# Performance work log

Hardware: AMD Instinct MI355X
Metric: run time of the kernel (lower is better)

## Reference

```python
import jax, jax.numpy as jnp
import numpy as np
from jax import lax

CHUNK = 64
EPS = 1e-5


def chunk_gla(q, k, v, g, chunk=CHUNK):
    """Gated linear attention, chunked parallel form (scale=1, as in HGRN2).
    q,k,g: [B,H,L,DK]; v: [B,H,L,DV]; g is per-step log decay on key dims.
    Recurrence: S_t = diag(exp(g_t)) S_{t-1} + k_t^T v_t ; o_t = q_t S_t.
    """
    B, H, L, DK = q.shape
    DV = v.shape[-1]
    n = L // chunk
    qc = q.reshape(B, H, n, chunk, DK)
    kc = k.reshape(B, H, n, chunk, DK)
    vc = v.reshape(B, H, n, chunk, DV)
    gc = jnp.cumsum(g.reshape(B, H, n, chunk, DK), axis=3)   # inclusive cumsum of log decays
    g_last = gc[..., -1:, :]                                 # [B,H,n,1,DK] total chunk decay

    qg = qc * jnp.exp(gc)                 # decay-weighted queries
    kg = kc * jnp.exp(g_last - gc)        # keys scaled to end-of-chunk
    kd = kc * jnp.exp(-gc)                # keys unscaled for intra-chunk attn

    # intra-chunk causal attention
    A = jnp.einsum('bhntd,bhnsd->bhnts', qg, kd)
    mask = jnp.tril(jnp.ones((chunk, chunk), dtype=bool))
    A = jnp.where(mask, A, 0.0)
    o_intra = jnp.einsum('bhnts,bhnsd->bhntd', A, vc)

    # inter-chunk recurrence over n chunks
    def step(S, inp):
        qg_c, kg_c, vc_c, gl_c = inp  # [B,H,C,DK], [B,H,C,DK], [B,H,C,DV], [B,H,DK]
        o = jnp.einsum('bhtd,bhdv->bhtv', qg_c, S)
        S = S * jnp.exp(gl_c)[..., None] + jnp.einsum('bhtd,bhtv->bhdv', kg_c, vc_c)
        return S, o

    S0 = jnp.zeros((B, H, DK, DV), q.dtype)
    xs = (jnp.moveaxis(qg, 2, 0), jnp.moveaxis(kg, 2, 0),
          jnp.moveaxis(vc, 2, 0), jnp.moveaxis(g_last[..., 0, :], 2, 0))
    _, o_inter = lax.scan(step, S0, xs)   # [n,B,H,C,DV]
    o = o_intra + jnp.moveaxis(o_inter, 0, 2)
    return o.reshape(B, H, L, DV)


def rms_norm(x, w, eps=EPS):
    var = jnp.mean(jnp.square(x), axis=-1, keepdims=True)
    return x * lax.rsqrt(var + eps) * w


def setup_inputs() -> dict:
    key = jax.random.key(0)
    B, L, D = 4, 2048, 2048
    ks = jax.random.split(key, 6)
    s = 1.0 / np.sqrt(D)
    return {
        'x': jax.random.normal(ks[0], (B, L, D), jnp.float32),
        'Wq': jax.random.normal(ks[1], (D, D), jnp.float32) * s,
        'Wf': jax.random.normal(ks[2], (D, D), jnp.float32) * s,
        'Wi': jax.random.normal(ks[3], (D, D), jnp.float32) * s,
        'Wo': jax.random.normal(ks[4], (D, D), jnp.float32) * s,
        'gnorm_w': jnp.ones((D,), jnp.float32),
    }


def reference(x, Wq, Wf, Wi, Wo, gnorm_w):
    B, L, D = x.shape
    H = 16
    Dh = D // H

    q = jax.nn.sigmoid(x @ Wq.T)
    f = jax.nn.sigmoid(x @ Wf.T)
    i = x @ Wi.T
    k = 1.0 - f
    g = jnp.log(f)

    def split_heads(t):  # b l (h d) -> b h l d
        return t.reshape(B, L, H, Dh).transpose(0, 2, 1, 3)

    q, k, i, g = map(split_heads, (q, k, i, g))
    o = chunk_gla(q, k, i, g)                  # [B,H,L,Dh]
    o = o.transpose(0, 2, 1, 3).reshape(B, L, D)
    o = rms_norm(o, gnorm_w)
    return o @ Wo.T
```

## Files before the change

kernel.cpp:

```cpp
#include <hip/hip_runtime.h>
#include <math.h>

typedef __bf16 bf16_t;
typedef __bf16 bf16x8 __attribute__((ext_vector_type(8)));
typedef float  f32x4  __attribute__((ext_vector_type(4)));

__device__ __forceinline__ void gl2lds16(const void* g, void* l) {
  __builtin_amdgcn_global_load_lds((__attribute__((address_space(1))) void*)g,
                                   (__attribute__((address_space(3))) void*)l,
                                   16, 0, 0);
}

template<int MODE>
__global__ __launch_bounds__(256, 2)
void gemm_bt(const bf16_t* __restrict__ A, const bf16_t* __restrict__ B,
             void* __restrict__ out0, float* __restrict__ out1,
             int M, int N, int K)
{
  __shared__ __align__(16) bf16_t As[128 * 32];
  __shared__ __align__(16) bf16_t Bs[128 * 32];
  const int tt   = threadIdx.x;
  const int wave = tt >> 6;
  const int lane = tt & 63;
  const int nblk = N >> 7;
  const int m0 = (int)(blockIdx.x / nblk) * 128;
  const int n0 = (int)(blockIdx.x % nblk) * 128;
  const int wr = (wave >> 1) * 64;
  const int wc = (wave & 1) * 64;
  const int r  = lane & 15;
  const int ko = (lane >> 4) * 8;
  const int c0 = tt, c1 = tt + 256;
  const int ar0 = c0 >> 2, ac0 = (c0 & 3) * 8;
  const int ar1 = c1 >> 2, ac1 = (c1 & 3) * 8;

  f32x4 acc[4][4] = {};

  for (int kt = 0; kt < K; kt += 32) {
    gl2lds16(A + (size_t)(m0 + ar0) * K + kt + ac0, (void*)(As + wave * 512));
    gl2lds16(A + (size_t)(m0 + ar1) * K + kt + ac1, (void*)(As + 2048 + wave * 512));
    gl2lds16(B + (size_t)(n0 + ar0) * K + kt + ac0, (void*)(Bs + wave * 512));
    gl2lds16(B + (size_t)(n0 + ar1) * K + kt + ac1, (void*)(Bs + 2048 + wave * 512));
    asm volatile("s_waitcnt vmcnt(0)" ::: "memory");
    __syncthreads();
    bf16x8 a[4], b[4];
    #pragma unroll
    for (int i = 0; i < 4; i++) a[i] = *(const bf16x8*)(As + (wr + i * 16 + r) * 32 + ko);
    #pragma unroll
    for (int i = 0; i < 4; i++) b[i] = *(const bf16x8*)(Bs + (wc + i * 16 + r) * 32 + ko);
    #pragma unroll
    for (int i = 0; i < 4; i++)
      #pragma unroll
      for (int j = 0; j < 4; j++)
        acc[i][j] = __builtin_amdgcn_mfma_f32_16x16x32_bf16(a[i], b[j], acc[i][j], 0, 0, 0);
    __syncthreads();
  }

  #pragma unroll
  for (int i = 0; i < 4; i++)
    #pragma unroll
    for (int j = 0; j < 4; j++)
      #pragma unroll
      for (int jj = 0; jj < 4; jj++) {
        const int gr = m0 + wr + i * 16 + (lane >> 4) * 4 + jj;
        const int gc = n0 + wc + j * 16 + r;
        const size_t off = (size_t)gr * N + gc;
        const float v = acc[i][j][jj];
        if (MODE == 0) {
          ((bf16_t*)out0)[off] = (bf16_t)(1.0f / (1.0f + expf(-v)));
        } else if (MODE == 1) {
          ((bf16_t*)out0)[off] = (bf16_t)(1.0f / (1.0f + expf(v)));
          out1[off] = fminf(v, 0.0f) - log1pf(expf(-fabsf(v)));
        } else if (MODE == 2) {
          ((bf16_t*)out0)[off] = (bf16_t)v;
        } else {
          ((float*)out0)[off] = v;
        }
      }
}

__global__ void f2b_kernel(const float* __restrict__ in, bf16_t* __restrict__ out, int n8)
{
  const int idx = blockIdx.x * 256 + threadIdx.x;
  if (idx >= n8) return;
  const float4 a = *(const float4*)(in + (size_t)idx * 8);
  const float4 b = *(const float4*)(in + (size_t)idx * 8 + 4);
  bf16x8 o;
  o[0] = (bf16_t)a.x; o[1] = (bf16_t)a.y; o[2] = (bf16_t)a.z; o[3] = (bf16_t)a.w;
  o[4] = (bf16_t)b.x; o[5] = (bf16_t)b.y; o[6] = (bf16_t)b.z; o[7] = (bf16_t)b.w;
  *(bf16x8*)(out + (size_t)idx * 8) = o;
}

__global__ __launch_bounds__(256)
void prep2_kernel(bf16_t* __restrict__ qb, bf16_t* __restrict__ kb,
                  const float* __restrict__ g32, float* __restrict__ eglh)
{
  __shared__ __align__(16) float gs[64][132];
  __shared__ float gls[128];
  const int blk = blockIdx.x;
  const int c = blk & 31, h = (blk >> 5) & 15, b = blk >> 9;
  const size_t row0 = (size_t)b * 2048 + (size_t)c * 64;
  const int col0 = h * 128;
  const int tt = threadIdx.x;

  #pragma unroll
  for (int s = 0; s < 8; s++) {
    const int u = tt + s * 256;
    const int t = u >> 5, d4 = (u & 31) * 4;
    *(float4*)&gs[t][d4] = *(const float4*)(g32 + (row0 + t) * 2048 + col0 + d4);
  }
  __syncthreads();
  if (tt < 128) {
    float run = 0.0f;
    for (int t = 0; t < 64; t++) { run += gs[t][tt]; gs[t][tt] = run; }
    gls[tt] = 0.5f * run;
    eglh[(size_t)blk * 128 + tt] = expf(0.5f * run);
  }
  __syncthreads();
  #pragma unroll
  for (int s = 0; s < 4; s++) {
    const int u = tt + s * 256;
    const int t = u >> 4, d8 = (u & 15) * 8;
    bf16_t* qp = qb + (row0 + t) * 2048 + col0 + d8;
    bf16_t* kp = kb + (row0 + t) * 2048 + col0 + d8;
    const bf16x8 q8 = *(const bf16x8*)qp;
    const bf16x8 k8 = *(const bf16x8*)kp;
    bf16x8 qo, ko2;
    #pragma unroll
    for (int j = 0; j < 8; j++) {
      const float gc = gs[t][d8 + j];
      const float gh = gls[d8 + j];
      qo[j]  = (bf16_t)((float)q8[j] * expf(gc - gh));
      ko2[j] = (bf16_t)((float)k8[j] * expf(gh - gc));
    }
    *(bf16x8*)qp = qo;
    *(bf16x8*)kp = ko2;
  }
}

__global__ __launch_bounds__(256)
void state2_kernel(const bf16_t* __restrict__ kb, const bf16_t* __restrict__ vb,
                   const float* __restrict__ eglh, bf16_t* __restrict__ ST)
{
  __shared__ __align__(16) bf16_t kgt[64][72];
  __shared__ __align__(16) bf16_t vt[64][72];
  __shared__ float ehs[64];
  const int blk = blockIdx.x;
  const int dh = blk & 1, eh = (blk >> 1) & 1, bh = blk >> 2;
  const int b = bh >> 4, h = bh & 15;
  const int col0 = h * 128;
  const int tt = threadIdx.x, wave = tt >> 6, lane = tt & 63;
  const int r = lane & 15, ko = (lane >> 4) * 8;
  const int d0 = dh * 64, e0 = eh * 64;
  f32x4 acc[4] = {};

  for (int c = 0; c < 32; c++) {
    const size_t cb = (size_t)bh * 32 + c;
    const size_t row0 = (size_t)b * 2048 + (size_t)c * 64;
    if (tt < 64) ehs[tt] = eglh[cb * 128 + d0 + tt];
    __syncthreads();
    #pragma unroll
    for (int s = 0; s < 2; s++) {
      const int u = tt + s * 256;
      const int t = u >> 3, d8 = (u & 7) * 8;
      const bf16x8 kv = *(const bf16x8*)(kb + (row0 + t) * 2048 + col0 + d0 + d8);
      const bf16x8 vv = *(const bf16x8*)(vb + (row0 + t) * 2048 + col0 + e0 + d8);
      #pragma unroll
      for (int j = 0; j < 8; j++) {
        kgt[d8 + j][t] = (bf16_t)((float)kv[j] * ehs[d8 + j]);
        vt[d8 + j][t]  = vv[j];
      }
    }
    __syncthreads();
    #pragma unroll
    for (int nf = 0; nf < 4; nf++) {
      const int d = nf * 16 + r;
      const float sd = ehs[d];
      #pragma unroll
      for (int jj = 0; jj < 4; jj++) {
        const int e = e0 + wave * 16 + (lane >> 4) * 4 + jj;
        ST[(cb * 128 + e) * 128 + d0 + d] = (bf16_t)(acc[nf][jj] * sd);
      }
    }
    #pragma unroll
    for (int nf = 0; nf < 4; nf++) {
      const float ev = ehs[nf * 16 + r];
      const float e2 = ev * ev;
      #pragma unroll
      for (int jj = 0; jj < 4; jj++) acc[nf][jj] *= e2;
    }
    #pragma unroll
    for (int ks = 0; ks < 2; ks++) {
      const bf16x8 a = *(const bf16x8*)&vt[wave * 16 + r][ks * 32 + ko];
      #pragma unroll
      for (int nf = 0; nf < 4; nf++) {
        const bf16x8 bfr = *(const bf16x8*)&kgt[nf * 16 + r][ks * 32 + ko];
        acc[nf] = __builtin_amdgcn_mfma_f32_16x16x32_bf16(a, bfr, acc[nf], 0, 0, 0);
      }
    }
    __syncthreads();
  }
}

__global__ __launch_bounds__(256)
void chunk2_kernel(const bf16_t* __restrict__ qb, const bf16_t* __restrict__ kb,
                   const bf16_t* __restrict__ vb, const bf16_t* __restrict__ ST,
                   bf16_t* __restrict__ o16)
{
  __shared__ __align__(16) bf16_t qgs[64][136];
  __shared__ __align__(16) bf16_t kds[64][136];
  __shared__ __align__(16) bf16_t vTs[128][72];
  __shared__ __align__(16) bf16_t Ps[64][72];
  const int blk = blockIdx.x;
  const int c = blk & 31, h = (blk >> 5) & 15, b = blk >> 9;
  const size_t row0 = (size_t)b * 2048 + (size_t)c * 64;
  const int col0 = h * 128;
  const int tt = threadIdx.x, wave = tt >> 6, lane = tt & 63;
  const int r = lane & 15, ko = (lane >> 4) * 8;

  #pragma unroll
  for (int s = 0; s < 4; s++) {
    const int u = tt + s * 256;
    const int t = u >> 4, d8 = (u & 15) * 8;
    *(bf16x8*)&qgs[t][d8] = *(const bf16x8*)(qb + (row0 + t) * 2048 + col0 + d8);
    *(bf16x8*)&kds[t][d8] = *(const bf16x8*)(kb + (row0 + t) * 2048 + col0 + d8);
  }
  #pragma unroll
  for (int s = 0; s < 4; s++) {
    const int u = tt + s * 256;
    const int t = u >> 4, e8 = (u & 15) * 8;
    const bf16x8 vv = *(const bf16x8*)(vb + (row0 + t) * 2048 + col0 + e8);
    #pragma unroll
    for (int j = 0; j < 8; j++) vTs[e8 + j][t] = vv[j];
  }
  __syncthreads();

  bf16x8 aq[4];
  #pragma unroll
  for (int ks = 0; ks < 4; ks++) aq[ks] = *(const bf16x8*)&qgs[wave * 16 + r][ks * 32 + ko];

  f32x4 accA[4] = {};
  #pragma unroll
  for (int ks = 0; ks < 4; ks++)
    #pragma unroll
    for (int sf = 0; sf < 4; sf++) {
      const bf16x8 bfr = *(const bf16x8*)&kds[sf * 16 + r][ks * 32 + ko];
      accA[sf] = __builtin_amdgcn_mfma_f32_16x16x32_bf16(aq[ks], bfr, accA[sf], 0, 0, 0);
    }

  #pragma unroll
  for (int sf = 0; sf < 4; sf++)
    #pragma unroll
    for (int jj = 0; jj < 4; jj++) {
      const int t = wave * 16 + (lane >> 4) * 4 + jj;
      const int s = sf * 16 + r;
      Ps[t][s] = (bf16_t)(t >= s ? accA[sf][jj] : 0.0f);
    }

  f32x4 acc[8] = {};
  const size_t stbase = (size_t)blk * 128 * 128;
  #pragma unroll
  for (int ks = 0; ks < 4; ks++)
    #pragma unroll
    for (int ne = 0; ne < 8; ne++) {
      const bf16x8 bfr = *(const bf16x8*)(ST + stbase + (size_t)(ne * 16 + r) * 128 + ks * 32 + ko);
      acc[ne] = __builtin_amdgcn_mfma_f32_16x16x32_bf16(aq[ks], bfr, acc[ne], 0, 0, 0);
    }
  #pragma unroll
  for (int ks = 0; ks < 2; ks++) {
    const bf16x8 pa = *(const bf16x8*)&Ps[wave * 16 + r][ks * 32 + ko];
    #pragma unroll
    for (int ne = 0; ne < 8; ne++) {
      const bf16x8 bfr = *(const bf16x8*)&vTs[ne * 16 + r][ks * 32 + ko];
      acc[ne] = __builtin_amdgcn_mfma_f32_16x16x32_bf16(pa, bfr, acc[ne], 0, 0, 0);
    }
  }

  #pragma unroll
  for (int ne = 0; ne < 8; ne++)
    #pragma unroll
    for (int jj = 0; jj < 4; jj++) {
      const int t = wave * 16 + (lane >> 4) * 4 + jj;
      const int e = ne * 16 + r;
      o16[(row0 + t) * 2048 + col0 + e] = (bf16_t)acc[ne][jj];
    }
}

__global__ __launch_bounds__(256)
void rmsb_kernel(const bf16_t* __restrict__ o16, const float* __restrict__ w,
                 bf16_t* __restrict__ ob)
{
  __shared__ float red[4];
  const size_t row = blockIdx.x;
  const int tt = threadIdx.x;
  const bf16x8 v = *(const bf16x8*)(o16 + row * 2048 + tt * 8);
  float f[8], ss = 0.0f;
  #pragma unroll
  for (int j = 0; j < 8; j++) { f[j] = (float)v[j]; ss += f[j] * f[j]; }
  #pragma unroll
  for (int off = 32; off > 0; off >>= 1) ss += __shfl_down(ss, off);
  if ((tt & 63) == 0) red[tt >> 6] = ss;
  __syncthreads();
  const float inv = rsqrtf((red[0] + red[1] + red[2] + red[3]) * (1.0f / 2048.0f) + 1e-5f);
  const float4 w0 = *(const float4*)(w + tt * 8);
  const float4 w1 = *(const float4*)(w + tt * 8 + 4);
  bf16x8 o;
  o[0] = (bf16_t)(f[0] * inv * w0.x); o[1] = (bf16_t)(f[1] * inv * w0.y);
  o[2] = (bf16_t)(f[2] * inv * w0.z); o[3] = (bf16_t)(f[3] * inv * w0.w);
  o[4] = (bf16_t)(f[4] * inv * w1.x); o[5] = (bf16_t)(f[5] * inv * w1.y);
  o[6] = (bf16_t)(f[6] * inv * w1.z); o[7] = (bf16_t)(f[7] * inv * w1.w);
  *(bf16x8*)(ob + row * 2048 + tt * 8) = o;
}

extern "C" void kernel_launch(void* const* d_in, const int* in_sizes, int n_in,
                              void* d_out, int out_size, void* d_ws, size_t ws_size,
                              hipStream_t stream)
{
  const float* x  = (const float*)d_in[0];
  const float* Wq = (const float*)d_in[1];
  const float* Wf = (const float*)d_in[2];
  const float* Wi = (const float*)d_in[3];
  const float* Wo = (const float*)d_in[4];
  const float* gw = (const float*)d_in[5];
  float* out = (float*)d_out;
  char* ws = (char*)d_ws;

  const int N = 2048, K = 2048;
  const size_t MB = 1ull << 20;

  auto run = [&](const float* xs, float* outs, int nbs) {
    const int Ms = nbs * 2048;
    const size_t Sx = (size_t)Ms * 2048 * 2;
    bf16_t* xb  = (bf16_t*)(ws + 0);
    bf16_t* qb  = (bf16_t*)(ws + Sx);
    bf16_t* kb  = (bf16_t*)(ws + 2 * Sx);
    bf16_t* vb  = (bf16_t*)(ws + 3 * Sx);
    float*  g32 = (float*) (ws + 4 * Sx);
    bf16_t* Wb  = (bf16_t*)(ws + 6 * Sx);
    float*  egh = (float*) (ws + 6 * Sx + 8 * MB);
    bf16_t* STp = (bf16_t*)(ws + 4 * Sx);
    bf16_t* o16 = (bf16_t*)(ws + 0);
    bf16_t* ob  = (bf16_t*)(ws + Sx);

    const int n8x = Ms * 2048 / 8;
    const int n8w = N * K / 8;
    const int gemmGrid = (Ms / 128) * (N / 128);

    f2b_kernel<<<(n8x + 255) / 256, 256, 0, stream>>>(xs, xb, n8x);

    f2b_kernel<<<(n8w + 255) / 256, 256, 0, stream>>>(Wq, Wb, n8w);
    gemm_bt<0><<<gemmGrid, 256, 0, stream>>>(xb, Wb, qb, nullptr, Ms, N, K);

    f2b_kernel<<<(n8w + 255) / 256, 256, 0, stream>>>(Wf, Wb, n8w);
    gemm_bt<1><<<gemmGrid, 256, 0, stream>>>(xb, Wb, kb, g32, Ms, N, K);

    f2b_kernel<<<(n8w + 255) / 256, 256, 0, stream>>>(Wi, Wb, n8w);
    gemm_bt<2><<<gemmGrid, 256, 0, stream>>>(xb, Wb, vb, nullptr, Ms, N, K);

    prep2_kernel<<<nbs * 512, 256, 0, stream>>>(qb, kb, g32, egh);
    state2_kernel<<<nbs * 64, 256, 0, stream>>>(kb, vb, egh, STp);
    chunk2_kernel<<<nbs * 512, 256, 0, stream>>>(qb, kb, vb, STp, o16);
    rmsb_kernel<<<Ms, 256, 0, stream>>>(o16, gw, ob);

    f2b_kernel<<<(n8w + 255) / 256, 256, 0, stream>>>(Wo, Wb, n8w);
    gemm_bt<3><<<gemmGrid, 256, 0, stream>>>(ob, Wb, outs, nullptr, Ms, N, K);
  };

  const size_t Sx_full = (size_t)8192 * 2048 * 2;
  const size_t need_full = 6 * Sx_full + 8 * MB + 4 * 512 * 128 * 4;
  if (ws_size >= need_full) {
    run(x, out, 4);
  } else {
    for (int sb = 0; sb < 4; sb++)
      run(x + (size_t)sb * 2048 * 2048, out + (size_t)sb * 2048 * 2048, 1);
  }

  (void)in_sizes; (void)n_in; (void)out_size;
}
```

Measured before the change: 679.9 us.

## Fuse Q/F/I projections into one 256x256-tile double-buffered GEMM

Replaces the 128x128 single-buffered GEMM with a 256x256 tile, 512-thread kernel that uses 64-wide K steps, XOR-swizzled LDS, double-buffered global-to-LDS loads and setprio around MFMA bursts. The three input projections are concatenated into one N=6144 GEMM whose epilogue dispatches per 2048-column segment, so the activations are read once and there is a single launch. The aim is more data reuse per LDS load, load/compute overlap and fewer kernel launches. In exchange it needs 128KB of dynamic LDS at one block per CU and a larger weight workspace.

```diff
diff --git a/kernel.cpp b/kernel.cpp
--- a/kernel.cpp
+++ b/kernel.cpp
@@ -11,71 +11,125 @@
                                    16, 0, 0);
 }
 
+#define MFMA16(a, b, c) __builtin_amdgcn_mfma_f32_16x16x32_bf16(a, b, c, 0, 0, 0)
+
 template<int MODE>
-__global__ __launch_bounds__(256, 2)
-void gemm_bt(const bf16_t* __restrict__ A, const bf16_t* __restrict__ B,
-             void* __restrict__ out0, float* __restrict__ out1,
-             int M, int N, int K)
-{
-  __shared__ __align__(16) bf16_t As[128 * 32];
-  __shared__ __align__(16) bf16_t Bs[128 * 32];
-  const int tt   = threadIdx.x;
-  const int wave = tt >> 6;
-  const int lane = tt & 63;
-  const int nblk = N >> 7;
-  const int m0 = (int)(blockIdx.x / nblk) * 128;
-  const int n0 = (int)(blockIdx.x % nblk) * 128;
-  const int wr = (wave >> 1) * 64;
-  const int wc = (wave & 1) * 64;
-  const int r  = lane & 15;
-  const int ko = (lane >> 4) * 8;
-  const int c0 = tt, c1 = tt + 256;
-  const int ar0 = c0 >> 2, ac0 = (c0 & 3) * 8;
-  const int ar1 = c1 >> 2, ac1 = (c1 & 3) * 8;
-
-  f32x4 acc[4][4] = {};
-
-  for (int kt = 0; kt < K; kt += 32) {
-    gl2lds16(A + (size_t)(m0 + ar0) * K + kt + ac0, (void*)(As + wave * 512));
-    gl2lds16(A + (size_t)(m0 + ar1) * K + kt + ac1, (void*)(As + 2048 + wave * 512));
-    gl2lds16(B + (size_t)(n0 + ar0) * K + kt + ac0, (void*)(Bs + wave * 512));
-    gl2lds16(B + (size_t)(n0 + ar1) * K + kt + ac1, (void*)(Bs + 2048 + wave * 512));
+__global__ __launch_bounds__(512, 1)
+void gemm256(const bf16_t* __restrict__ A, const bf16_t* __restrict__ Bw,
+             bf16_t* __restrict__ oq, bf16_t* __restrict__ okk,
+             bf16_t* __restrict__ ov, float* __restrict__ og,
+             float* __restrict__ of, int M, int N, int K)
+{
+  extern __shared__ __align__(16) char smem[];
+  const int tt = threadIdx.x;
+  const int wave = tt >> 6, lane = tt & 63;
+  const int wm = wave >> 2, wn = wave & 3;
+  const int nbn = N >> 8;
+  const int m0 = (int)(blockIdx.x / nbn) << 8;
+  const int n0 = (int)(blockIdx.x % nbn) << 8;
+  const int l15 = lane & 15, lq = lane >> 4;
+
+  const int tk0 = (lq * 16) ^ ((lane & 7) << 4);
+  const int tk1 = (64 + lq * 16) ^ ((lane & 7) << 4);
+  const int aRow = (wm * 128 + l15) * 128;
+  const int bRow = (wn * 64  + l15) * 128;
+
+  const int srow = tt >> 3;
+  const int scol = ((tt & 7) * 8) ^ ((srow & 7) * 8);
+  const bf16_t* pA = A  + (size_t)(m0 + srow) * K + scol;
+  const bf16_t* pB = Bw + (size_t)(n0 + srow) * K + scol;
+  const size_t rstep = (size_t)64 * K;
+
+  f32x4 acc[8][4] = {};
+  const int T = K >> 6;
+
+  auto stage = [&](int t, int s) {
+    const int kt = t << 6;
+    char* da = smem + s * 32768 + wave * 1024;
+    char* db = smem + 65536 + s * 32768 + wave * 1024;
+    #pragma unroll
+    for (int i = 0; i < 4; i++) {
+      gl2lds16(pA + i * rstep + kt, da + i * 8192);
+      gl2lds16(pB + i * rstep + kt, db + i * 8192);
+    }
+  };
+
+  stage(0, 0);
+  asm volatile("s_waitcnt vmcnt(0)" ::: "memory");
+  __builtin_amdgcn_s_barrier();
+
+  for (int t = 0; t < T; t++) {
+    const int s = t & 1;
+    if (t + 1 < T) stage(t + 1, s ^ 1);
+    const char* as = smem + s * 32768;
+    const char* bs = smem + 65536 + s * 32768;
+    bf16x8 bfr[4][2];
+    #pragma unroll
+    for (int nf = 0; nf < 4; nf++) {
+      bfr[nf][0] = *(const bf16x8*)(bs + bRow + nf * 2048 + tk0);
+      bfr[nf][1] = *(const bf16x8*)(bs + bRow + nf * 2048 + tk1);
+    }
+    #pragma unroll
+    for (int q = 0; q < 4; q++) {
+      bf16x8 af[2][2];
+      #pragma unroll
+      for (int mm = 0; mm < 2; mm++) {
+        af[mm][0] = *(const bf16x8*)(as + aRow + (q * 2 + mm) * 2048 + tk0);
+        af[mm][1] = *(const bf16x8*)(as + aRow + (q * 2 + mm) * 2048 + tk1);
+      }
+      __builtin_amdgcn_s_barrier();
+      asm volatile("s_waitcnt lgkmcnt(0)" ::: "memory");
+      __builtin_amdgcn_sched_barrier(0);
+      __builtin_amdgcn_s_setprio(1);
+      #pragma unroll
+      for (int mm = 0; mm < 2; mm++)
+        #pragma unroll
+        for (int nf = 0; nf < 4; nf++) {
+          acc[q * 2 + mm][nf] = MFMA16(af[mm][0], bfr[nf][0], acc[q * 2 + mm][nf]);
+          acc[q * 2 + mm][nf] = MFMA16(af[mm][1], bfr[nf][1], acc[q * 2 + mm][nf]);
+        }
+      __builtin_amdgcn_s_setprio(0);
+      if (q < 3) __builtin_amdgcn_s_barrier();
+    }
     asm volatile("s_waitcnt vmcnt(0)" ::: "memory");
-    __syncthreads();
-    bf16x8 a[4], b[4];
-    #pragma unroll
-    for (int i = 0; i < 4; i++) a[i] = *(const bf16x8*)(As + (wr + i * 16 + r) * 32 + ko);
-    #pragma unroll
-    for (int i = 0; i < 4; i++) b[i] = *(const bf16x8*)(Bs + (wc + i * 16 + r) * 32 + ko);
-    #pragma unroll
-    for (int i = 0; i < 4; i++)
-      #pragma unroll
-      for (int j = 0; j < 4; j++)
-        acc[i][j] = __builtin_amdgcn_mfma_f32_16x16x32_bf16(a[i], b[j], acc[i][j], 0, 0, 0);
-    __syncthreads();
-  }
-
-  #pragma unroll
-  for (int i = 0; i < 4; i++)
-    #pragma unroll
-    for (int j = 0; j < 4; j++)
-      #pragma unroll
-      for (int jj = 0; jj < 4; jj++) {
-        const int gr = m0 + wr + i * 16 + (lane >> 4) * 4 + jj;
-        const int gc = n0 + wc + j * 16 + r;
-        const size_t off = (size_t)gr * N + gc;
-        const float v = acc[i][j][jj];
-        if (MODE == 0) {
-          ((bf16_t*)out0)[off] = (bf16_t)(1.0f / (1.0f + expf(-v)));
-        } else if (MODE == 1) {
-          ((bf16_t*)out0)[off] = (bf16_t)(1.0f / (1.0f + expf(v)));
-          out1[off] = fminf(v, 0.0f) - log1pf(expf(-fabsf(v)));
-        } else if (MODE == 2) {
-          ((bf16_t*)out0)[off] = (bf16_t)v;
-        } else {
-          ((float*)out0)[off] = v;
+    __builtin_amdgcn_s_barrier();
+  }
+
+  const int er = lq * 4;
+  if (MODE == 0) {
+    const int seg = n0 >> 11;
+    const int gc = (n0 & 2047) + wn * 64 + l15;
+    #pragma unroll
+    for (int mf = 0; mf < 8; mf++)
+      #pragma unroll
+      for (int nf = 0; nf < 4; nf++) {
+        const int gr = m0 + wm * 128 + mf * 16 + er;
+        #pragma unroll
+        for (int jj = 0; jj < 4; jj++) {
+          const size_t off = (size_t)(gr + jj) * 2048 + gc + nf * 16;
+          const float v = acc[mf][nf][jj];
+          if (seg == 0) {
+            oq[off] = (bf16_t)(1.0f / (1.0f + expf(-v)));
+          } else if (seg == 1) {
+            okk[off] = (bf16_t)(1.0f / (1.0f + expf(v)));
+            og[off] = fminf(v, 0.0f) - log1pf(expf(-fabsf(v)));
+          } else {
+            ov[off] = (bf16_t)v;
+          }
         }
       }
+  } else {
+    const int gc = n0 + wn * 64 + l15;
+    #pragma unroll
+    for (int mf = 0; mf < 8; mf++)
+      #pragma unroll
+      for (int nf = 0; nf < 4; nf++) {
+        const int gr = m0 + wm * 128 + mf * 16 + er;
+        #pragma unroll
+        for (int jj = 0; jj < 4; jj++)
+          of[(size_t)(gr + jj) * N + gc + nf * 16] = acc[mf][nf][jj];
+      }
+  }
 }
 
 __global__ void f2b_kernel(const float* __restrict__ in, bf16_t* __restrict__ out, int n8)
@@ -194,7 +248,7 @@
       #pragma unroll
       for (int nf = 0; nf < 4; nf++) {
         const bf16x8 bfr = *(const bf16x8*)&kgt[nf * 16 + r][ks * 32 + ko];
-        acc[nf] = __builtin_amdgcn_mfma_f32_16x16x32_bf16(a, bfr, acc[nf], 0, 0, 0);
+        acc[nf] = MFMA16(a, bfr, acc[nf]);
       }
     }
     __syncthreads();
@@ -244,7 +298,7 @@
     #pragma unroll
     for (int sf = 0; sf < 4; sf++) {
       const bf16x8 bfr = *(const bf16x8*)&kds[sf * 16 + r][ks * 32 + ko];
-      accA[sf] = __builtin_amdgcn_mfma_f32_16x16x32_bf16(aq[ks], bfr, accA[sf], 0, 0, 0);
+      accA[sf] = MFMA16(aq[ks], bfr, accA[sf]);
     }
 
   #pragma unroll
@@ -263,7 +317,7 @@
     #pragma unroll
     for (int ne = 0; ne < 8; ne++) {
       const bf16x8 bfr = *(const bf16x8*)(ST + stbase + (size_t)(ne * 16 + r) * 128 + ks * 32 + ko);
-      acc[ne] = __builtin_amdgcn_mfma_f32_16x16x32_bf16(aq[ks], bfr, acc[ne], 0, 0, 0);
+      acc[ne] = MFMA16(aq[ks], bfr, acc[ne]);
     }
   #pragma unroll
   for (int ks = 0; ks < 2; ks++) {
@@ -271,7 +325,7 @@
     #pragma unroll
     for (int ne = 0; ne < 8; ne++) {
       const bf16x8 bfr = *(const bf16x8*)&vTs[ne * 16 + r][ks * 32 + ko];
-      acc[ne] = __builtin_amdgcn_mfma_f32_16x16x32_bf16(pa, bfr, acc[ne], 0, 0, 0);
+      acc[ne] = MFMA16(pa, bfr, acc[ne]);
     }
   }
 
@@ -324,8 +378,14 @@
   float* out = (float*)d_out;
   char* ws = (char*)d_ws;
 
-  const int N = 2048, K = 2048;
+  const int K = 2048;
   const size_t MB = 1ull << 20;
+  const int LDS = 131072;
+
+  (void)hipFuncSetAttribute((const void*)gemm256<0>,
+      hipFuncAttributeMaxDynamicSharedMemorySize, LDS);
+  (void)hipFuncSetAttribute((const void*)gemm256<1>,
+      hipFuncAttributeMaxDynamicSharedMemorySize, LDS);
 
   auto run = [&](const float* xs, float* outs, int nbs) {
     const int Ms = nbs * 2048;
@@ -336,25 +396,21 @@
     bf16_t* vb  = (bf16_t*)(ws + 3 * Sx);
     float*  g32 = (float*) (ws + 4 * Sx);
     bf16_t* Wb  = (bf16_t*)(ws + 6 * Sx);
-    float*  egh = (float*) (ws + 6 * Sx + 8 * MB);
+    float*  egh = (float*) (ws + 6 * Sx + 24 * MB);
     bf16_t* STp = (bf16_t*)(ws + 4 * Sx);
     bf16_t* o16 = (bf16_t*)(ws + 0);
     bf16_t* ob  = (bf16_t*)(ws + Sx);
 
     const int n8x = Ms * 2048 / 8;
-    const int n8w = N * K / 8;
-    const int gemmGrid = (Ms / 128) * (N / 128);
+    const int n8w = 2048 * 2048 / 8;
 
     f2b_kernel<<<(n8x + 255) / 256, 256, 0, stream>>>(xs, xb, n8x);
-
     f2b_kernel<<<(n8w + 255) / 256, 256, 0, stream>>>(Wq, Wb, n8w);
-    gemm_bt<0><<<gemmGrid, 256, 0, stream>>>(xb, Wb, qb, nullptr, Ms, N, K);
-
-    f2b_kernel<<<(n8w + 255) / 256, 256, 0, stream>>>(Wf, Wb, n8w);
-    gemm_bt<1><<<gemmGrid, 256, 0, stream>>>(xb, Wb, kb, g32, Ms, N, K);
-
-    f2b_kernel<<<(n8w + 255) / 256, 256, 0, stream>>>(Wi, Wb, n8w);
-    gemm_bt<2><<<gemmGrid, 256, 0, stream>>>(xb, Wb, vb, nullptr, Ms, N, K);
+    f2b_kernel<<<(n8w + 255) / 256, 256, 0, stream>>>(Wf, Wb + 4194304, n8w);
+    f2b_kernel<<<(n8w + 255) / 256, 256, 0, stream>>>(Wi, Wb + 8388608, n8w);
+
+    gemm256<0><<<(Ms / 256) * (6144 / 256), 512, LDS, stream>>>(
+        xb, Wb, qb, kb, vb, g32, nullptr, Ms, 6144, K);
 
     prep2_kernel<<<nbs * 512, 256, 0, stream>>>(qb, kb, g32, egh);
     state2_kernel<<<nbs * 64, 256, 0, stream>>>(kb, vb, egh, STp);
@@ -362,11 +418,12 @@
     rmsb_kernel<<<Ms, 256, 0, stream>>>(o16, gw, ob);
 
     f2b_kernel<<<(n8w + 255) / 256, 256, 0, stream>>>(Wo, Wb, n8w);
-    gemm_bt<3><<<gemmGrid, 256, 0, stream>>>(ob, Wb, outs, nullptr, Ms, N, K);
+    gemm256<1><<<(Ms / 256) * (2048 / 256), 512, LDS, stream>>>(
+        ob, Wb, nullptr, nullptr, nullptr, nullptr, outs, Ms, 2048, K);
   };
 
   const size_t Sx_full = (size_t)8192 * 2048 * 2;
-  const size_t need_full = 6 * Sx_full + 8 * MB + 4 * 512 * 128 * 4;
+  const size_t need_full = 6 * Sx_full + 24 * MB + 2048 * 128 * 4;
   if (ws_size >= need_full) {
     run(x, out, 4);
   } else {
```

Result: slower. 874.4 us (+28.6%).
